# Performance work log

Measured on AMD Instinct MI355X. Metric: run time of the kernel, lower is better.

The kernel has to match this reference:

```python
import jax, jax.numpy as jnp
from jax import lax
import numpy as np


def _conv(x, w, b, pad):
    y = lax.conv_general_dilated(x, w, (1, 1), [(pad, pad), (pad, pad)],
                                 dimension_numbers=('NCHW', 'OIHW', 'NCHW'))
    return y + b[None, :, None, None]


def _bn(x, g, b, eps=1e-5):
    # training-mode batchnorm (batch statistics, biased variance) like torch default
    m = jnp.mean(x, (0, 2, 3), keepdims=True)
    v = jnp.mean((x - m) ** 2, (0, 2, 3), keepdims=True)
    return g[None, :, None, None] * (x - m) * lax.rsqrt(v + eps) + b[None, :, None, None]


def _maxpool2(x):
    return lax.reduce_window(x, -jnp.inf, lax.max, (1, 1, 2, 2), (1, 1, 2, 2), 'VALID')


def _power_features(x):
    # vectorized version of the per-image FFT + radial-bin histogram mean
    B, _, H, W = x.shape
    cy, cx = H // 2, W // 2
    yy, xx = jnp.meshgrid(jnp.arange(H), jnp.arange(W), indexing='ij')
    r = jnp.sqrt((xx - cx).astype(jnp.float32) ** 2 + (yy - cy).astype(jnp.float32) ** 2)
    max_r = min(H, W) // 2
    NB = 32
    r_bins = jnp.linspace(0.0, float(max_r), NB + 1)
    # bin j covers [r_bins[j], r_bins[j+1]) exactly as the torch mask
    idx = jnp.searchsorted(r_bins, r.ravel(), side='right') - 1
    valid = (idx >= 0) & (idx < NB)
    seg = jnp.where(valid, idx, NB)  # dump out-of-range into bin NB
    counts = jax.ops.segment_sum(valid.astype(jnp.float32), seg, NB + 1)[:NB]
    ps = jnp.abs(jnp.fft.fft2(x[:, 0])) ** 2  # [B,H,W]
    psf = ps.reshape(B, -1) * valid.astype(ps.dtype)[None, :]
    sums = jax.vmap(lambda p: jax.ops.segment_sum(p, seg, NB + 1))(psf)[:, :NB]
    radial = jnp.where(counts > 0, sums / jnp.maximum(counts, 1.0), 0.0)
    return jnp.log(radial + 1e-10)  # [B,32]


def reference(x, cw1, cb1, g1, bb1, cw2, cb2, g2, bb2, cw3, cb3, g3, bb3,
              cw4, cb4, g4, bb4, pcw, pcb, pg, pbb,
              pw1, pb1, pw2, pb2, pw3, pb3,
              fw1, fb1, fw2, fb2, fw3, fb3, fw4, fb4):
    h = jax.nn.relu(_bn(_conv(x, cw1, cb1, 2), g1, bb1)); h = _maxpool2(h)
    h = jax.nn.relu(_bn(_conv(h, cw2, cb2, 2), g2, bb2)); h = _maxpool2(h)
    h = jax.nn.relu(_bn(_conv(h, cw3, cb3, 1), g3, bb3)); h = _maxpool2(h)
    h = jax.nn.relu(_bn(_conv(h, cw4, cb4, 1), g4, bb4))        # [B,256,32,32]
    p = jax.nn.relu(_bn(_conv(h, pcw, pcb, 1), pg, pbb))        # [B,128,32,32]
    # adaptive avg pool (4,4): exact 8x8 windows, stride 8
    p = lax.reduce_window(p, 0.0, lax.add, (1, 1, 8, 8), (1, 1, 8, 8), 'VALID') / 64.0
    flat = p.reshape(p.shape[0], -1)  # [B,2048]
    pf = _power_features(x)           # [B,32]
    pf = jax.nn.relu(pf @ pw1.T + pb1)
    pf = jax.nn.relu(pf @ pw2.T + pb2)
    pf = jax.nn.relu(pf @ pw3.T + pb3)  # [B,64]
    c = jnp.concatenate([flat, pf], axis=1)  # [B,2112]
    c = jax.nn.relu(c @ fw1.T + fb1)
    c = jax.nn.relu(c @ fw2.T + fb2)
    c = jax.nn.relu(c @ fw3.T + fb3)
    return c @ fw4.T + fb4  # [B,2]


def setup_inputs() -> dict:
    key = jax.random.key(0)
    ki = iter(jax.random.split(key, 40))

    def W(shape):
        fan_in = int(np.prod(shape[1:]))
        return jax.random.normal(next(ki), shape, jnp.float32) / np.sqrt(fan_in)

    d = {'x': jax.random.normal(next(ki), (16, 1, 256, 256), jnp.float32)}
    convs = [('cw1', 'cb1', 'g1', 'bb1', (32, 1, 5, 5)),
             ('cw2', 'cb2', 'g2', 'bb2', (64, 32, 5, 5)),
             ('cw3', 'cb3', 'g3', 'bb3', (128, 64, 3, 3)),
             ('cw4', 'cb4', 'g4', 'bb4', (256, 128, 3, 3)),
             ('pcw', 'pcb', 'pg', 'pbb', (128, 256, 3, 3))]
    for wn, bn, gn, ben, s in convs:
        d[wn] = W(s); d[bn] = jnp.zeros(s[0], jnp.float32)
        d[gn] = jnp.ones(s[0], jnp.float32); d[ben] = jnp.zeros(s[0], jnp.float32)
    lins = [('pw1', 'pb1', (256, 32)), ('pw2', 'pb2', (128, 256)), ('pw3', 'pb3', (64, 128)),
            ('fw1', 'fb1', (512, 2112)), ('fw2', 'fb2', (256, 512)),
            ('fw3', 'fb3', (128, 256)), ('fw4', 'fb4', (2, 128))]
    for wn, bn, s in lins:
        d[wn] = W(s); d[bn] = jnp.zeros(s[0], jnp.float32)
    return d
```

## Files before the change

kernel.cpp:

```cpp
#include <hip/hip_runtime.h>
#include <math.h>


#define PI2F 6.283185307179586f

typedef _Float16 half8 __attribute__((ext_vector_type(8)));
typedef _Float16 half4v __attribute__((ext_vector_type(4)));
typedef float f32x4 __attribute__((ext_vector_type(4)));


__device__ __forceinline__ int bitrev8(int x) {
  x = ((x & 0x0F) << 4) | ((x >> 4) & 0x0F);
  x = ((x & 0x33) << 2) | ((x >> 2) & 0x33);
  x = ((x & 0x55) << 1) | ((x >> 1) & 0x55);
  return x;
}

__global__ __launch_bounds__(64)
void fft_rows(const float* __restrict__ x, float2* __restrict__ out) {
  __shared__ float2 s[256];
  __shared__ float2 tw[128];
  int blk = blockIdx.x;
  const float* rowp = x + (size_t)blk * 256;
  int t = threadIdx.x;
  for (int i = t; i < 128; i += 64) {
    float sn, cs;
    sincosf(-(PI2F / 256.f) * (float)i, &sn, &cs);
    tw[i] = make_float2(cs, sn);
  }
  #pragma unroll
  for (int e = 0; e < 4; ++e) {
    int i = t + (e << 6);
    s[bitrev8(i)] = make_float2(rowp[i], 0.f);
  }
  __syncthreads();
  #pragma unroll
  for (int st = 1; st <= 8; ++st) {
    int half = 1 << (st - 1);
    #pragma unroll
    for (int j = 0; j < 2; ++j) {
      int bf = t + (j << 6);
      int pos = bf & (half - 1);
      int grp = bf >> (st - 1);
      int i0 = (grp << st) | pos;
      int i1 = i0 + half;
      int k = pos << (8 - st);
      float cs = tw[k].x, sn = tw[k].y;
      float2 a = s[i0], b = s[i1];
      float tr = cs * b.x - sn * b.y;
      float ti = cs * b.y + sn * b.x;
      s[i0] = make_float2(a.x + tr, a.y + ti);
      s[i1] = make_float2(a.x - tr, a.y - ti);
    }
    __syncthreads();
  }
  float2* op = out + (size_t)blk * 256;
  #pragma unroll
  for (int e = 0; e < 4; ++e) { int i = t + (e << 6); op[i] = s[i]; }
}

__device__ __forceinline__ int radial_bin(int r2) {
  int j = (int)(sqrtf((float)r2) * 0.25f);
  while ((j + 1) * (j + 1) * 16 <= r2) ++j;
  while (j > 0 && j * j * 16 > r2) --j;
  return j;
}

__global__ __launch_bounds__(256)
void fft_cols_radial_v2(const float2* __restrict__ f, float* __restrict__ radial) {
  __shared__ float2 s[8][258];
  __shared__ float2 tw[128];
  __shared__ float bins[8][32];
  int b = blockIdx.x >> 5;
  int col0 = (blockIdx.x & 31) * 8;
  int t = threadIdx.x;
  for (int i = t; i < 128; i += 256) {
    float sn, cs;
    sincosf(-(PI2F / 256.f) * (float)i, &sn, &cs);
    tw[i] = make_float2(cs, sn);
  }
  ((float*)bins)[t] = 0.f;
  for (int idx = t; idx < 2048; idx += 256) {
    int row = idx >> 3, c = idx & 7;
    s[c][bitrev8(row)] = f[(size_t)b * 65536 + row * 256 + col0 + c];
  }
  __syncthreads();
  int c = t >> 5, l = t & 31;
  float2* sc = &s[c][0];
  #pragma unroll
  for (int st = 1; st <= 8; ++st) {
    int half = 1 << (st - 1);
    #pragma unroll
    for (int j = 0; j < 4; ++j) {
      int bf = l + (j << 5);
      int pos = bf & (half - 1);
      int grp = bf >> (st - 1);
      int i0 = (grp << st) | pos;
      int i1 = i0 + half;
      int k = pos << (8 - st);
      float cs = tw[k].x, sn = tw[k].y;
      float2 a = sc[i0], bb = sc[i1];
      float tr = cs * bb.x - sn * bb.y;
      float ti = cs * bb.y + sn * bb.x;
      sc[i0] = make_float2(a.x + tr, a.y + ti);
      sc[i1] = make_float2(a.x - tr, a.y - ti);
    }
    __syncthreads();
  }
  int dx = col0 + c - 128;
  #pragma unroll
  for (int e = 0; e < 8; ++e) {
    int i = l * 8 + e;
    float2 v = sc[i];
    float ps = v.x * v.x + v.y * v.y;
    int dy = i - 128;
    int r2 = dx * dx + dy * dy;
    if (r2 < 16384) atomicAdd(&bins[c][radial_bin(r2)], ps);
  }
  __syncthreads();
  if (t < 32) {
    float s0 = bins[0][t] + bins[1][t] + bins[2][t] + bins[3][t] +
               bins[4][t] + bins[5][t] + bins[6][t] + bins[7][t];
    atomicAdd(&radial[b * 32 + t], s0);
  }
}

__device__ __forceinline__ int isqrt_(int v) {
  int r = (int)sqrtf((float)v);
  while (r * r > v) --r;
  while ((r + 1) * (r + 1) <= v) ++r;
  return r;
}

__global__ __launch_bounds__(256)
void radial_finalize_v3(const float* __restrict__ radial, float* __restrict__ pf0) {
  __shared__ int red[4];
  __shared__ int cnt_s;
  int j = blockIdx.x, t = threadIdx.x;
  int dy = t - 128;
  int lo = 16 * j * j, hi = 16 * (j + 1) * (j + 1);
  int d2 = dy * dy;
  int cnt = 0;
  int tHi = hi - 1 - d2;
  if (tHi >= 0) {
    int rHi = isqrt_(tHi);
    int nHi = min(rHi, 127) + min(rHi, 128) + 1;
    int nLo = 0;
    int tLo = lo - 1 - d2;
    if (tLo >= 0) { int rLo = isqrt_(tLo); nLo = min(rLo, 127) + min(rLo, 128) + 1; }
    cnt = nHi - nLo;
  }
  #pragma unroll
  for (int off = 32; off > 0; off >>= 1) cnt += __shfl_down(cnt, off);
  if ((t & 63) == 0) red[t >> 6] = cnt;
  __syncthreads();
  if (t == 0) cnt_s = red[0] + red[1] + red[2] + red[3];
  __syncthreads();
  if (t < 16) {
    float cf = (float)cnt_s;
    float sum = radial[t * 32 + j];
    float val = cf > 0.f ? sum / fmaxf(cf, 1.f) : 0.f;
    pf0[t * 32 + j] = logf(val + 1e-10f);
  }
}


__global__ __launch_bounds__(256)
void wtrans_all(const float* __restrict__ cw2, const float* __restrict__ cw3,
                const float* __restrict__ cw4, const float* __restrict__ pcw,
                _Float16* __restrict__ wb2, _Float16* __restrict__ wb3,
                _Float16* __restrict__ wb4, _Float16* __restrict__ wbp) {
  int blk = blockIdx.x;
  const float* src; _Float16* dst; int COUT, CIN, KK, i;
  if (blk < 200)       { src = cw2; dst = wb2; COUT = 64;  CIN = 32;  KK = 25; i = blk * 256; }
  else if (blk < 488)  { src = cw3; dst = wb3; COUT = 128; CIN = 64;  KK = 9;  i = (blk - 200) * 256; }
  else if (blk < 1640) { src = cw4; dst = wb4; COUT = 256; CIN = 128; KK = 9;  i = (blk - 488) * 256; }
  else                 { src = pcw; dst = wbp; COUT = 128; CIN = 256; KK = 9;  i = (blk - 1640) * 256; }
  i += threadIdx.x;
  if (i >= COUT * CIN * KK) return;
  int ci = i % CIN;
  int r = i / CIN;
  int co = r % COUT;
  int tap = r / COUT;
  dst[i] = (_Float16)src[((size_t)co * CIN + ci) * KK + tap];
}


__device__ __forceinline__ void load16(float* d, const float* p) {
  f32x4 v0 = *(const f32x4*)(p);
  f32x4 v1 = *(const f32x4*)(p + 4);
  f32x4 v2 = *(const f32x4*)(p + 8);
  f32x4 v3 = *(const f32x4*)(p + 12);
  #pragma unroll
  for (int e = 0; e < 4; ++e) { d[e] = v0[e]; d[4+e] = v1[e]; d[8+e] = v2[e]; d[12+e] = v3[e]; }
}

__global__ __launch_bounds__(256)
void conv1_stats_v3(const float* __restrict__ x, const float* __restrict__ w,
                    float* __restrict__ stats) {
  __shared__ float lds[12 * 264];
  __shared__ float r1[4][32], r2[4][32];
  int t = threadIdx.x;
  int y0 = blockIdx.x * 8, n = blockIdx.y;
  const float* xp = x + (size_t)n * 65536;
  for (int i = t; i < 12 * 264; i += 256) {
    int r = i / 264, cc = i % 264;
    int gy = y0 + r - 2, gx = cc - 4;
    lds[i] = (gy >= 0 && gy < 256 && gx >= 0 && gx < 256) ? xp[gy * 256 + gx] : 0.f;
  }
  __syncthreads();
  int c = t & 31, xg = t >> 5;
  float wreg[25];
  #pragma unroll
  for (int k = 0; k < 25; ++k) wreg[k] = w[c * 25 + k];
  float s1 = 0.f, s2 = 0.f;
  for (int strip = 0; strip < 4; ++strip) {
    int px0 = xg * 8 + strip * 64;
    float f[5][16];
    #pragma unroll
    for (int rr = 0; rr < 4; ++rr) load16(f[rr], &lds[rr * 264 + px0]);
    #pragma unroll
    for (int r = 0; r < 8; ++r) {
      load16(f[(r + 4) % 5], &lds[(r + 4) * 264 + px0]);
      f32x4 A = {0.f, 0.f, 0.f, 0.f}, B = {0.f, 0.f, 0.f, 0.f};
      #pragma unroll
      for (int ky = 0; ky < 5; ++ky) {
        const float* fr = f[(r + ky) % 5];
        #pragma unroll
        for (int kx = 0; kx < 5; ++kx) {
          float wv = wreg[ky * 5 + kx];
          f32x4 ia = {fr[2 + kx], fr[3 + kx], fr[4 + kx], fr[5 + kx]};
          f32x4 ib = {fr[6 + kx], fr[7 + kx], fr[8 + kx], fr[9 + kx]};
          A += wv * ia; B += wv * ib;
        }
      }
      s1 += A[0] + A[1] + A[2] + A[3] + B[0] + B[1] + B[2] + B[3];
      s2 += A[0]*A[0] + A[1]*A[1] + A[2]*A[2] + A[3]*A[3]
          + B[0]*B[0] + B[1]*B[1] + B[2]*B[2] + B[3]*B[3];
    }
  }
  s1 += __shfl_down(s1, 32);
  s2 += __shfl_down(s2, 32);
  if ((t & 63) < 32) { r1[t >> 6][t & 31] = s1; r2[t >> 6][t & 31] = s2; }
  __syncthreads();
  if (t < 32) {
    atomicAdd(&stats[t],      r1[0][t] + r1[1][t] + r1[2][t] + r1[3][t]);
    atomicAdd(&stats[32 + t], r2[0][t] + r2[1][t] + r2[2][t] + r2[3][t]);
  }
}

__global__ __launch_bounds__(256)
void conv1_apply_v3(const float* __restrict__ x, const float* __restrict__ w,
                    const float* __restrict__ stats, const float* __restrict__ g,
                    const float* __restrict__ bb, _Float16* __restrict__ pool1) {
  __shared__ float lds[6 * 264];
  int t = threadIdx.x;
  int py = blockIdx.x, n = blockIdx.y;
  const float* xp = x + (size_t)n * 65536;
  for (int i = t; i < 6 * 264; i += 256) {
    int r = i / 264, cc = i % 264;
    int gy = 2 * py + r - 2, gx = cc - 4;
    lds[i] = (gy >= 0 && gy < 256 && gx >= 0 && gx < 256) ? xp[gy * 256 + gx] : 0.f;
  }
  __syncthreads();
  int c = t & 31, xg = t >> 5;
  float wreg[25];
  #pragma unroll
  for (int k = 0; k < 25; ++k) wreg[k] = w[c * 25 + k];
  float mean = stats[c] * (1.f / 1048576.f);
  float var  = stats[32 + c] * (1.f / 1048576.f) - mean * mean;
  float sc = g[c] / sqrtf(var + 1e-5f);
  float sh = bb[c] - mean * sc;
  for (int iter = 0; iter < 4; ++iter) {
    int p0 = xg * 4 + iter * 32;
    float f[6][16];
    #pragma unroll
    for (int rr = 0; rr < 6; ++rr) load16(f[rr], &lds[rr * 264 + 2 * p0]);
    f32x4 acc[2][2];
    #pragma unroll
    for (int sy = 0; sy < 2; ++sy)
      #pragma unroll
      for (int h = 0; h < 2; ++h) acc[sy][h] = (f32x4){0.f, 0.f, 0.f, 0.f};
    #pragma unroll
    for (int sy = 0; sy < 2; ++sy)
      #pragma unroll
      for (int ky = 0; ky < 5; ++ky) {
        const float* fr = f[sy + ky];
        #pragma unroll
        for (int kx = 0; kx < 5; ++kx) {
          float wv = wreg[ky * 5 + kx];
          f32x4 ia = {fr[2 + kx], fr[3 + kx], fr[4 + kx], fr[5 + kx]};
          f32x4 ib = {fr[6 + kx], fr[7 + kx], fr[8 + kx], fr[9 + kx]};
          acc[sy][0] += wv * ia; acc[sy][1] += wv * ib;
        }
      }
    #pragma unroll
    for (int pp = 0; pp < 4; ++pp) {
      float v00 = acc[0][(2*pp) >> 2][(2*pp) & 3];
      float v01 = acc[0][(2*pp+1) >> 2][(2*pp+1) & 3];
      float v10 = acc[1][(2*pp) >> 2][(2*pp) & 3];
      float v11 = acc[1][(2*pp+1) >> 2][(2*pp+1) & 3];
      float m = fmaxf(fmaxf(v00, v01), fmaxf(v10, v11));
      pool1[(((size_t)n * 128 + py) * 128 + p0 + pp) * 32 + c] =
          (_Float16)fmaxf(m * sc + sh, 0.f);
    }
  }
}


template <int CIN, int COUT, int H, int W, int K, int TH, int TW, int CW,
          int COT, int PT, int SLAB, int POOL>
__global__ __launch_bounds__(256)
void conv_mfma3(const _Float16* __restrict__ in, const _Float16* __restrict__ wb,
                _Float16* __restrict__ out, float* __restrict__ stats,
                size_t minoff) {
  constexpr int P = K / 2, R = TH + 2 * P, XW = TW + 2 * P, PIX = R * XW;
  constexpr int TAPS = K * K, CSP = SLAB + 8;
  constexpr int NCC = SLAB / 32, NPH = CIN / SLAB, SUBS = SLAB / 8;
  constexpr int PW = 4 / CW, COB = CW * 16 * COT;
  static_assert(TH * TW == PW * 16 * PT, "pos tile mismatch");
  static_assert(TW == 16, "row-per-fragment requires TW=16");
  static_assert(!POOL || (PT % 2 == 0), "pool needs even PT");
  __shared__ _Float16 lds[PIX * CSP];
  __shared__ float sst[2][COB];
  int t = threadIdx.x;
  int lane = t & 63, wv = t >> 6;
  int lane15 = lane & 15, quad = lane >> 4;
  constexpr int WT = W / TW;
  int x0 = (blockIdx.x % WT) * TW, y0 = (blockIdx.x / WT) * TH;
  int coB = blockIdx.y * COB;
  int nb = blockIdx.z;
  int co_off = (wv % CW) * (16 * COT);
  int rowbase = (wv / CW) * PT;

  for (int i = t; i < 2 * COB; i += 256) ((float*)sst)[i] = 0.f;

  f32x4 acc[COT][PT];
  #pragma unroll
  for (int ct = 0; ct < COT; ++ct)
    #pragma unroll
    for (int pt = 0; pt < PT; ++pt)
      #pragma unroll
      for (int e = 0; e < 4; ++e) acc[ct][pt][e] = 0.f;

  int bbase[PT];
  #pragma unroll
  for (int pt = 0; pt < PT; ++pt)
    bbase[pt] = ((rowbase + pt) * XW + lane15) * CSP + quad * 8;
  const _Float16* aptr[COT];
  #pragma unroll
  for (int ct = 0; ct < COT; ++ct)
    aptr[ct] = wb + (size_t)(coB + co_off + ct * 16 + lane15) * CIN + quad * 8;

  const _Float16* inb = in + (size_t)nb * H * W * CIN;

  #pragma unroll
  for (int ph = 0; ph < NPH; ++ph) {
    constexpr int ITEMS = PIX * SUBS;
    for (int i = t; i < ITEMS; i += 256) {
      int sub = i % SUBS, pix = i / SUBS;
      int r = pix / XW, xx = pix % XW;
      int gy = y0 + r - P, gx = x0 + xx - P;
      half8 v;
      #pragma unroll
      for (int j = 0; j < 8; ++j) v[j] = (_Float16)0.f;
      if (gy >= 0 && gy < H && gx >= 0 && gx < W)
        v = *(const half8*)(inb + ((size_t)gy * W + gx) * CIN + ph * SLAB + sub * 8);
      *(half8*)(&lds[pix * CSP + sub * 8]) = v;
    }
    __syncthreads();
    #pragma unroll
    for (int cc = 0; cc < NCC; ++cc) {
      #pragma unroll
      for (int tap = 0; tap < TAPS; ++tap) {
        int ky = tap / K, kx = tap % K;
        half8 a[COT], b[PT];
        #pragma unroll
        for (int ct = 0; ct < COT; ++ct)
          a[ct] = *(const half8*)(aptr[ct] + (size_t)tap * COUT * CIN +
                                  ph * SLAB + cc * 32);
        #pragma unroll
        for (int pt = 0; pt < PT; ++pt)
          b[pt] = *(const half8*)(&lds[bbase[pt] + (ky * XW + kx) * CSP + cc * 32]);
        #pragma unroll
        for (int ct = 0; ct < COT; ++ct)
          #pragma unroll
          for (int pt = 0; pt < PT; ++pt)
            acc[ct][pt] = __builtin_amdgcn_mfma_f32_16x16x32_f16(
                a[ct], b[pt], acc[ct][pt], 0, 0, 0);
      }
    }
    if (ph + 1 < NPH) __syncthreads();
  }

  if (POOL) {
    #pragma unroll
    for (int ct = 0; ct < COT; ++ct)
      #pragma unroll
      for (int pp = 0; pp < PT; pp += 2) {
        half4v hmax, hmin;
        #pragma unroll
        for (int e = 0; e < 4; ++e) {
          float vmx = fmaxf(acc[ct][pp][e], acc[ct][pp + 1][e]);
          float vmn = fminf(acc[ct][pp][e], acc[ct][pp + 1][e]);
          float omx = fmaxf(vmx, __shfl_xor(vmx, 1));
          float omn = fminf(vmn, __shfl_xor(vmn, 1));
          hmax[e] = (_Float16)omx; hmin[e] = (_Float16)omn;
        }
        if ((lane15 & 1) == 0) {
          int co = coB + co_off + ct * 16 + quad * 4;
          int prow = (y0 + rowbase + pp) >> 1;
          int pcol = (x0 >> 1) + (lane15 >> 1);
          size_t idx = (((size_t)nb * (H / 2) + prow) * (W / 2) + pcol) * COUT + co;
          *(half4v*)(out + idx) = hmax;
          *(half4v*)(out + minoff + idx) = hmin;
        }
      }
  } else {
    #pragma unroll
    for (int ct = 0; ct < COT; ++ct)
      #pragma unroll
      for (int pt = 0; pt < PT; ++pt) {
        int co = coB + co_off + ct * 16 + quad * 4;
        int y = y0 + rowbase + pt, x = x0 + lane15;
        _Float16* op = out + (((size_t)nb * H + y) * W + x) * COUT + co;
        half4v h;
        #pragma unroll
        for (int e = 0; e < 4; ++e) h[e] = (_Float16)acc[ct][pt][e];
        *(half4v*)op = h;
      }
  }

  #pragma unroll
  for (int ct = 0; ct < COT; ++ct)
    #pragma unroll
    for (int e = 0; e < 4; ++e) {
      float sv = 0.f, sq = 0.f;
      #pragma unroll
      for (int pt = 0; pt < PT; ++pt) {
        float v = acc[ct][pt][e];
        sv += v; sq += v * v;
      }
      sv += __shfl_xor(sv, 1); sq += __shfl_xor(sq, 1);
      sv += __shfl_xor(sv, 2); sq += __shfl_xor(sq, 2);
      sv += __shfl_xor(sv, 4); sq += __shfl_xor(sq, 4);
      sv += __shfl_xor(sv, 8); sq += __shfl_xor(sq, 8);
      if (lane15 == 0) {
        int cl = co_off + ct * 16 + quad * 4 + e;
        atomicAdd(&sst[0][cl], sv);
        atomicAdd(&sst[1][cl], sq);
      }
    }
  __syncthreads();
  float* st = stats + (blockIdx.x & 7) * 2 * COUT;
  for (int i = t; i < COB; i += 256) {
    atomicAdd(&st[coB + i], sst[0][i]);
    atomicAdd(&st[COUT + coB + i], sst[1][i]);
  }
}


__device__ __forceinline__ void bn_coeff(const float* stats, int C, int c,
                                         float invN, const float* g,
                                         const float* bb, float* sc, float* sh) {
  float s1 = 0.f, s2 = 0.f;
  #pragma unroll
  for (int s = 0; s < 8; ++s) {
    s1 += stats[s * 2 * C + c];
    s2 += stats[s * 2 * C + C + c];
  }
  float mean = s1 * invN;
  float var  = s2 * invN - mean * mean;
  float k = g[c] / sqrtf(var + 1e-5f);
  *sc = k; *sh = bb[c] - mean * k;
}

__global__ __launch_bounds__(256)
void bn_relu_sel(const _Float16* __restrict__ raw, const float* __restrict__ stats,
                 const float* __restrict__ g, const float* __restrict__ bb,
                 _Float16* __restrict__ out, int C, int total, float invN,
                 size_t minoff) {
  __shared__ float scs[256], shs[256];
  int t = threadIdx.x, n = blockIdx.y;
  for (int c = t; c < C; c += 256) bn_coeff(stats, C, c, invN, g, bb, &scs[c], &shs[c]);
  __syncthreads();
  for (int i = blockIdx.x * 256 + t; i < total; i += gridDim.x * 256) {
    int c = i % C;
    size_t idx = (size_t)n * total + i;
    float sc = scs[c];
    float v = sc >= 0.f ? (float)raw[idx] : (float)raw[minoff + idx];
    out[idx] = (_Float16)fmaxf(sc * v + shs[c], 0.f);
  }
}

__global__ __launch_bounds__(256)
void bn_relu_h16(const _Float16* __restrict__ x, const float* __restrict__ stats,
                 const float* __restrict__ g, const float* __restrict__ bb,
                 _Float16* __restrict__ out, int C, int HW, float invN) {
  __shared__ float scs[256], shs[256];
  int t = threadIdx.x;
  int n = blockIdx.y;
  for (int c = t; c < C; c += 256) bn_coeff(stats, C, c, invN, g, bb, &scs[c], &shs[c]);
  __syncthreads();
  int total = HW * C;
  int chunk = total / gridDim.x;
  int base = blockIdx.x * chunk;
  const _Float16* xp = x + (size_t)n * total;
  _Float16* op = out + (size_t)n * total;
  for (int i = base + t; i < base + chunk; i += 256) {
    int c = i % C;
    op[i] = (_Float16)fmaxf((float)xp[i] * scs[c] + shs[c], 0.f);
  }
}

__global__ __launch_bounds__(256)
void bn_avgpool_concat(const _Float16* __restrict__ x, const float* __restrict__ stats,
                       const float* __restrict__ g, const float* __restrict__ bb,
                       float* __restrict__ concat, float invN) {
  __shared__ float scs[128], shs[128];
  int t = threadIdx.x;
  int n = blockIdx.x;
  for (int c = t; c < 128; c += 256) bn_coeff(stats, 128, c, invN, g, bb, &scs[c], &shs[c]);
  __syncthreads();
  for (int i = t; i < 2048; i += 256) {
    int c = i & 127, opix = i >> 7;
    int py = opix >> 2, px = opix & 3;
    float sc = scs[c], sh = shs[c];
    float s = 0.f;
    for (int yy = 0; yy < 8; ++yy)
      for (int xx = 0; xx < 8; ++xx)
        s += fmaxf((float)x[(((size_t)n * 32 + py * 8 + yy) * 32 + px * 8 + xx) * 128 + c] * sc + sh, 0.f);
    concat[(size_t)n * 2112 + c * 16 + opix] = s * (1.f / 64.f);
  }
}


__global__ __launch_bounds__(64)
void linear_k(const float* __restrict__ in, const float* __restrict__ w,
              const float* __restrict__ bias, float* __restrict__ out,
              int I, int in_stride, int out_stride, int relu) {
  int o = blockIdx.x, b = blockIdx.y;
  int lane = threadIdx.x;
  const float* ip = in + (size_t)b * in_stride;
  const float* wp = w + (size_t)o * I;
  float acc = 0.f;
  for (int i = lane; i < I; i += 64) acc += ip[i] * wp[i];
  #pragma unroll
  for (int off = 32; off > 0; off >>= 1) acc += __shfl_down(acc, off);
  if (lane == 0) {
    float v = acc + bias[o];
    if (relu) v = fmaxf(v, 0.f);
    out[(size_t)b * out_stride + o] = v;
  }
}

__global__ __launch_bounds__(256)
void pf_mlp(const float* __restrict__ pf0,
            const float* __restrict__ pw1, const float* __restrict__ pb1,
            const float* __restrict__ pw2, const float* __restrict__ pb2,
            const float* __restrict__ pw3, const float* __restrict__ pb3,
            float* __restrict__ concat) {
  __shared__ float a0[32], a1[256], a2[128];
  int b = blockIdx.x, t = threadIdx.x;
  if (t < 32) a0[t] = pf0[b * 32 + t];
  __syncthreads();
  {
    float s = pb1[t];
    for (int i = 0; i < 32; ++i) s += pw1[t * 32 + i] * a0[i];
    a1[t] = fmaxf(s, 0.f);
  }
  __syncthreads();
  if (t < 128) {
    float s = pb2[t];
    for (int i = 0; i < 256; ++i) s += pw2[t * 256 + i] * a1[i];
    a2[t] = fmaxf(s, 0.f);
  }
  __syncthreads();
  if (t < 64) {
    float s = pb3[t];
    for (int i = 0; i < 128; ++i) s += pw3[t * 128 + i] * a2[i];
    concat[(size_t)b * 2112 + 2048 + t] = fmaxf(s, 0.f);
  }
}

__global__ __launch_bounds__(256)
void fc_tail(const float* __restrict__ fc1o,
             const float* __restrict__ fw2, const float* __restrict__ fb2,
             const float* __restrict__ fw3, const float* __restrict__ fb3,
             const float* __restrict__ fw4, const float* __restrict__ fb4,
             float* __restrict__ out) {
  __shared__ float a1[512], a2[256], a3[128];
  int b = blockIdx.x, t = threadIdx.x;
  a1[t] = fc1o[b * 512 + t];
  a1[t + 256] = fc1o[b * 512 + t + 256];
  __syncthreads();
  {
    float s = fb2[t];
    for (int i = 0; i < 512; ++i) s += fw2[t * 512 + i] * a1[i];
    a2[t] = fmaxf(s, 0.f);
  }
  __syncthreads();
  if (t < 128) {
    float s = fb3[t];
    for (int i = 0; i < 256; ++i) s += fw3[t * 256 + i] * a2[i];
    a3[t] = fmaxf(s, 0.f);
  }
  __syncthreads();
  if (t < 2) {
    float s = fb4[t];
    for (int i = 0; i < 128; ++i) s += fw4[t * 128 + i] * a3[i];
    out[b * 2 + t] = s;
  }
}


extern "C" void kernel_launch(void* const* d_in, const int* in_sizes, int n_in,
                              void* d_out, int out_size, void* d_ws, size_t ws_size,
                              hipStream_t stream) {
  (void)in_sizes; (void)n_in; (void)out_size; (void)ws_size;
  const float* x   = (const float*)d_in[0];
  const float* cw1 = (const float*)d_in[1];
  const float* g1  = (const float*)d_in[3];
  const float* bb1 = (const float*)d_in[4];
  const float* cw2 = (const float*)d_in[5];
  const float* g2  = (const float*)d_in[7];
  const float* bb2 = (const float*)d_in[8];
  const float* cw3 = (const float*)d_in[9];
  const float* g3  = (const float*)d_in[11];
  const float* bb3 = (const float*)d_in[12];
  const float* cw4 = (const float*)d_in[13];
  const float* g4  = (const float*)d_in[15];
  const float* bb4 = (const float*)d_in[16];
  const float* pcw = (const float*)d_in[17];
  const float* pg  = (const float*)d_in[19];
  const float* pbb = (const float*)d_in[20];
  const float* pw1 = (const float*)d_in[21];
  const float* pb1 = (const float*)d_in[22];
  const float* pw2 = (const float*)d_in[23];
  const float* pb2 = (const float*)d_in[24];
  const float* pw3 = (const float*)d_in[25];
  const float* pb3 = (const float*)d_in[26];
  const float* fw1 = (const float*)d_in[27];
  const float* fb1 = (const float*)d_in[28];
  const float* fw2 = (const float*)d_in[29];
  const float* fb2 = (const float*)d_in[30];
  const float* fw3 = (const float*)d_in[31];
  const float* fb3 = (const float*)d_in[32];
  const float* fw4 = (const float*)d_in[33];
  const float* fb4 = (const float*)d_in[34];

  char* base = (char*)d_ws;
  float2*    fftbuf   = (float2*)(base + 0);
  _Float16*  pool2raw = (_Float16*)(base + 0);
  _Float16*  pool3raw = (_Float16*)(base + 0);
  _Float16*  conv4raw = (_Float16*)(base + 0);
  _Float16*  pconvo   = (_Float16*)(base + 8388608);
  _Float16*  pool1    = (_Float16*)(base + 16777216);
  _Float16*  pool2    = (_Float16*)(base + 33554432);
  _Float16*  pool3    = (_Float16*)(base + 41943040);
  _Float16*  act4     = (_Float16*)(base + 46137344);
  _Float16*  wb2      = (_Float16*)(base + 54525952);
  _Float16*  wb3      = (_Float16*)(base + 54628352);
  _Float16*  wb4      = (_Float16*)(base + 54775808);
  _Float16*  wbp      = (_Float16*)(base + 55365632);
  float*     zbase    = (float*)(base + 55955456);
  float*     stats1   = zbase;
  float*     stats2   = zbase + 64;
  float*     stats3   = zbase + 1088;
  float*     stats4   = zbase + 3136;
  float*     stats5   = zbase + 7232;
  float*     radial   = zbase + 9280;
  float*     pf0      = (float*)(base + 55994624);
  float*     concat   = (float*)(base + 55996672);
  float*     fc1o     = (float*)(base + 56131840);

  hipMemsetAsync(zbase, 0, 9792 * sizeof(float), stream);

  wtrans_all<<<2792, 256, 0, stream>>>(cw2, cw3, cw4, pcw, wb2, wb3, wb4, wbp);

  fft_rows<<<4096, 64, 0, stream>>>(x, fftbuf);
  fft_cols_radial_v2<<<512, 256, 0, stream>>>(fftbuf, radial);
  radial_finalize_v3<<<32, 256, 0, stream>>>(radial, pf0);
  pf_mlp<<<16, 256, 0, stream>>>(pf0, pw1, pb1, pw2, pb2, pw3, pb3, concat);

  conv1_stats_v3<<<dim3(32, 16), 256, 0, stream>>>(x, cw1, stats1);
  conv1_apply_v3<<<dim3(128, 16), 256, 0, stream>>>(x, cw1, stats1, g1, bb1, pool1);

  conv_mfma3<32, 64, 128, 128, 5, 16, 16, 1, 4, 4, 32, 1>
      <<<dim3(64, 1, 16), 256, 0, stream>>>(pool1, wb2, pool2raw, stats2, 4194304);
  bn_relu_sel<<<dim3(64, 16), 256, 0, stream>>>(
      pool2raw, stats2, g2, bb2, pool2, 64, 262144, 1.f / 262144.f, 4194304);

  conv_mfma3<64, 128, 64, 64, 3, 8, 16, 2, 4, 4, 64, 1>
      <<<dim3(32, 1, 16), 256, 0, stream>>>(pool2, wb3, pool3raw, stats3, 2097152);
  bn_relu_sel<<<dim3(32, 16), 256, 0, stream>>>(
      pool3raw, stats3, g3, bb3, pool3, 128, 131072, 1.f / 65536.f, 2097152);

  conv_mfma3<128, 256, 32, 32, 3, 4, 16, 2, 4, 2, 128, 0>
      <<<dim3(16, 2, 16), 256, 0, stream>>>(pool3, wb4, conv4raw, stats4, 0);
  bn_relu_h16<<<dim3(8, 16), 256, 0, stream>>>(
      conv4raw, stats4, g4, bb4, act4, 256, 1024, 1.f / 16384.f);

  conv_mfma3<256, 128, 32, 32, 3, 4, 16, 2, 2, 2, 128, 0>
      <<<dim3(16, 2, 16), 256, 0, stream>>>(act4, wbp, pconvo, stats5, 0);
  bn_avgpool_concat<<<16, 256, 0, stream>>>(pconvo, stats5, pg, pbb, concat, 1.f / 16384.f);

  linear_k<<<dim3(512, 16), 64, 0, stream>>>(concat, fw1, fb1, fc1o, 2112, 2112, 512, 1);
  fc_tail<<<16, 256, 0, stream>>>(fc1o, fw2, fb2, fw3, fb3, fw4, fb4, (float*)d_out);
}
```

Measured before the change: 466.9 us.

## Fuse BN-ReLU into next conv's input load and single-pass conv1 with max/min pooling

Conv1 is now computed once: its stats kernel also writes pooled max and min raw outputs, which replaces the separate apply pass that recomputed the convolution. Each MFMA conv applies the previous layer's batchnorm and ReLU while loading its input tile, choosing the max or min pooled value by the sign of the scale. This removes the standalone bn_relu kernels and their activation round trips through memory. Conv1 stats are split across 8 atomic slots to reduce contention. Some tile and grid shapes change (conv2 tile, conv4 COT), and bn_avgpool_concat is parallelised over more blocks. The cost is extra per-element BN math in the conv load path and a second min-buffer read.

```diff
diff --git a/kernel.cpp b/kernel.cpp
--- a/kernel.cpp
+++ b/kernel.cpp
@@ -196,8 +196,9 @@
 }
 
 __global__ __launch_bounds__(256)
-void conv1_stats_v3(const float* __restrict__ x, const float* __restrict__ w,
-                    float* __restrict__ stats) {
+void conv1_fused(const float* __restrict__ x, const float* __restrict__ w,
+                 _Float16* __restrict__ praw, size_t minoff,
+                 float* __restrict__ stats) {
   __shared__ float lds[12 * 264];
   __shared__ float r1[4][32], r2[4][32];
   int t = threadIdx.x;
@@ -219,6 +220,7 @@
     float f[5][16];
     #pragma unroll
     for (int rr = 0; rr < 4; ++rr) load16(f[rr], &lds[rr * 264 + px0]);
+    float pmax[4], pmin[4];
     #pragma unroll
     for (int r = 0; r < 8; ++r) {
       load16(f[(r + 4) % 5], &lds[(r + 4) * 264 + px0]);
@@ -237,6 +239,24 @@
       s1 += A[0] + A[1] + A[2] + A[3] + B[0] + B[1] + B[2] + B[3];
       s2 += A[0]*A[0] + A[1]*A[1] + A[2]*A[2] + A[3]*A[3]
           + B[0]*B[0] + B[1]*B[1] + B[2]*B[2] + B[3]*B[3];
+      float cm[4], cn[4];
+      cm[0] = fmaxf(A[0], A[1]); cn[0] = fminf(A[0], A[1]);
+      cm[1] = fmaxf(A[2], A[3]); cn[1] = fminf(A[2], A[3]);
+      cm[2] = fmaxf(B[0], B[1]); cn[2] = fminf(B[0], B[1]);
+      cm[3] = fmaxf(B[2], B[3]); cn[3] = fminf(B[2], B[3]);
+      if ((r & 1) == 0) {
+        #pragma unroll
+        for (int k = 0; k < 4; ++k) { pmax[k] = cm[k]; pmin[k] = cn[k]; }
+      } else {
+        int prow = (y0 + r) >> 1;
+        int pc0 = px0 >> 1;
+        #pragma unroll
+        for (int k = 0; k < 4; ++k) {
+          size_t idx = (((size_t)n * 128 + prow) * 128 + pc0 + k) * 32 + c;
+          praw[idx] = (_Float16)fmaxf(pmax[k], cm[k]);
+          praw[minoff + idx] = (_Float16)fminf(pmin[k], cn[k]);
+        }
+      }
     }
   }
   s1 += __shfl_down(s1, 32);
@@ -244,84 +264,31 @@
   if ((t & 63) < 32) { r1[t >> 6][t & 31] = s1; r2[t >> 6][t & 31] = s2; }
   __syncthreads();
   if (t < 32) {
-    atomicAdd(&stats[t],      r1[0][t] + r1[1][t] + r1[2][t] + r1[3][t]);
-    atomicAdd(&stats[32 + t], r2[0][t] + r2[1][t] + r2[2][t] + r2[3][t]);
-  }
-}
-
-__global__ __launch_bounds__(256)
-void conv1_apply_v3(const float* __restrict__ x, const float* __restrict__ w,
-                    const float* __restrict__ stats, const float* __restrict__ g,
-                    const float* __restrict__ bb, _Float16* __restrict__ pool1) {
-  __shared__ float lds[6 * 264];
-  int t = threadIdx.x;
-  int py = blockIdx.x, n = blockIdx.y;
-  const float* xp = x + (size_t)n * 65536;
-  for (int i = t; i < 6 * 264; i += 256) {
-    int r = i / 264, cc = i % 264;
-    int gy = 2 * py + r - 2, gx = cc - 4;
-    lds[i] = (gy >= 0 && gy < 256 && gx >= 0 && gx < 256) ? xp[gy * 256 + gx] : 0.f;
-  }
-  __syncthreads();
-  int c = t & 31, xg = t >> 5;
-  float wreg[25];
-  #pragma unroll
-  for (int k = 0; k < 25; ++k) wreg[k] = w[c * 25 + k];
-  float mean = stats[c] * (1.f / 1048576.f);
-  float var  = stats[32 + c] * (1.f / 1048576.f) - mean * mean;
-  float sc = g[c] / sqrtf(var + 1e-5f);
-  float sh = bb[c] - mean * sc;
-  for (int iter = 0; iter < 4; ++iter) {
-    int p0 = xg * 4 + iter * 32;
-    float f[6][16];
-    #pragma unroll
-    for (int rr = 0; rr < 6; ++rr) load16(f[rr], &lds[rr * 264 + 2 * p0]);
-    f32x4 acc[2][2];
-    #pragma unroll
-    for (int sy = 0; sy < 2; ++sy)
-      #pragma unroll
-      for (int h = 0; h < 2; ++h) acc[sy][h] = (f32x4){0.f, 0.f, 0.f, 0.f};
-    #pragma unroll
-    for (int sy = 0; sy < 2; ++sy)
-      #pragma unroll
-      for (int ky = 0; ky < 5; ++ky) {
-        const float* fr = f[sy + ky];
-        #pragma unroll
-        for (int kx = 0; kx < 5; ++kx) {
-          float wv = wreg[ky * 5 + kx];
-          f32x4 ia = {fr[2 + kx], fr[3 + kx], fr[4 + kx], fr[5 + kx]};
-          f32x4 ib = {fr[6 + kx], fr[7 + kx], fr[8 + kx], fr[9 + kx]};
-          acc[sy][0] += wv * ia; acc[sy][1] += wv * ib;
-        }
-      }
-    #pragma unroll
-    for (int pp = 0; pp < 4; ++pp) {
-      float v00 = acc[0][(2*pp) >> 2][(2*pp) & 3];
-      float v01 = acc[0][(2*pp+1) >> 2][(2*pp+1) & 3];
-      float v10 = acc[1][(2*pp) >> 2][(2*pp) & 3];
-      float v11 = acc[1][(2*pp+1) >> 2][(2*pp+1) & 3];
-      float m = fmaxf(fmaxf(v00, v01), fmaxf(v10, v11));
-      pool1[(((size_t)n * 128 + py) * 128 + p0 + pp) * 32 + c] =
-          (_Float16)fmaxf(m * sc + sh, 0.f);
-    }
+    float* st = stats + (blockIdx.x & 7) * 64;
+    atomicAdd(&st[t],      r1[0][t] + r1[1][t] + r1[2][t] + r1[3][t]);
+    atomicAdd(&st[32 + t], r2[0][t] + r2[1][t] + r2[2][t] + r2[3][t]);
   }
 }
 
 
 template <int CIN, int COUT, int H, int W, int K, int TH, int TW, int CW,
-          int COT, int PT, int SLAB, int POOL>
-__global__ __launch_bounds__(256)
-void conv_mfma3(const _Float16* __restrict__ in, const _Float16* __restrict__ wb,
-                _Float16* __restrict__ out, float* __restrict__ stats,
-                size_t minoff) {
+          int COT, int PT, int SLAB, int INPOOL, int OUTPOOL>
+__global__ __launch_bounds__(256)
+void conv_mfma4(const _Float16* __restrict__ in, size_t in_minoff,
+                const _Float16* __restrict__ wb,
+                _Float16* __restrict__ out, size_t out_minoff,
+                const float* __restrict__ instats, const float* __restrict__ ing,
+                const float* __restrict__ inbb, float in_invN,
+                float* __restrict__ stats) {
   constexpr int P = K / 2, R = TH + 2 * P, XW = TW + 2 * P, PIX = R * XW;
   constexpr int TAPS = K * K, CSP = SLAB + 8;
   constexpr int NCC = SLAB / 32, NPH = CIN / SLAB, SUBS = SLAB / 8;
   constexpr int PW = 4 / CW, COB = CW * 16 * COT;
   static_assert(TH * TW == PW * 16 * PT, "pos tile mismatch");
   static_assert(TW == 16, "row-per-fragment requires TW=16");
-  static_assert(!POOL || (PT % 2 == 0), "pool needs even PT");
+  static_assert(!OUTPOOL || (PT % 2 == 0), "pool needs even PT");
   __shared__ _Float16 lds[PIX * CSP];
+  __shared__ float inscs[CIN], inshs[CIN];
   __shared__ float sst[2][COB];
   int t = threadIdx.x;
   int lane = t & 63, wv = t >> 6;
@@ -334,6 +301,19 @@
   int rowbase = (wv / CW) * PT;
 
   for (int i = t; i < 2 * COB; i += 256) ((float*)sst)[i] = 0.f;
+  for (int c = t; c < CIN; c += 256) {
+    float s1 = 0.f, s2 = 0.f;
+    #pragma unroll
+    for (int s = 0; s < 8; ++s) {
+      s1 += instats[s * 2 * CIN + c];
+      s2 += instats[s * 2 * CIN + CIN + c];
+    }
+    float mean = s1 * in_invN;
+    float var  = s2 * in_invN - mean * mean;
+    float k = ing[c] / sqrtf(var + 1e-5f);
+    inscs[c] = k; inshs[c] = inbb[c] - mean * k;
+  }
+  __syncthreads();
 
   f32x4 acc[COT][PT];
   #pragma unroll
@@ -352,7 +332,7 @@
   for (int ct = 0; ct < COT; ++ct)
     aptr[ct] = wb + (size_t)(coB + co_off + ct * 16 + lane15) * CIN + quad * 8;
 
-  const _Float16* inb = in + (size_t)nb * H * W * CIN;
+  const size_t ibase = (size_t)nb * H * W * CIN;
 
   #pragma unroll
   for (int ph = 0; ph < NPH; ++ph) {
@@ -361,11 +341,29 @@
       int sub = i % SUBS, pix = i / SUBS;
       int r = pix / XW, xx = pix % XW;
       int gy = y0 + r - P, gx = x0 + xx - P;
+      int ch = ph * SLAB + sub * 8;
       half8 v;
       #pragma unroll
       for (int j = 0; j < 8; ++j) v[j] = (_Float16)0.f;
-      if (gy >= 0 && gy < H && gx >= 0 && gx < W)
-        v = *(const half8*)(inb + ((size_t)gy * W + gx) * CIN + ph * SLAB + sub * 8);
+      if (gy >= 0 && gy < H && gx >= 0 && gx < W) {
+        size_t off = ibase + ((size_t)gy * W + gx) * CIN + ch;
+        half8 vmx = *(const half8*)(in + off);
+        if (INPOOL) {
+          half8 vmn = *(const half8*)(in + in_minoff + off);
+          #pragma unroll
+          for (int j = 0; j < 8; ++j) {
+            float sc = inscs[ch + j];
+            float xv = sc >= 0.f ? (float)vmx[j] : (float)vmn[j];
+            v[j] = (_Float16)fmaxf(sc * xv + inshs[ch + j], 0.f);
+          }
+        } else {
+          #pragma unroll
+          for (int j = 0; j < 8; ++j) {
+            float sc = inscs[ch + j];
+            v[j] = (_Float16)fmaxf(sc * (float)vmx[j] + inshs[ch + j], 0.f);
+          }
+        }
+      }
       *(half8*)(&lds[pix * CSP + sub * 8]) = v;
     }
     __syncthreads();
@@ -393,7 +391,7 @@
     if (ph + 1 < NPH) __syncthreads();
   }
 
-  if (POOL) {
+  if (OUTPOOL) {
     #pragma unroll
     for (int ct = 0; ct < COT; ++ct)
       #pragma unroll
@@ -413,7 +411,7 @@
           int pcol = (x0 >> 1) + (lane15 >> 1);
           size_t idx = (((size_t)nb * (H / 2) + prow) * (W / 2) + pcol) * COUT + co;
           *(half4v*)(out + idx) = hmax;
-          *(half4v*)(out + minoff + idx) = hmin;
+          *(half4v*)(out + out_minoff + idx) = hmin;
         }
       }
   } else {
@@ -460,78 +458,36 @@
 }
 
 
-__device__ __forceinline__ void bn_coeff(const float* stats, int C, int c,
-                                         float invN, const float* g,
-                                         const float* bb, float* sc, float* sh) {
-  float s1 = 0.f, s2 = 0.f;
-  #pragma unroll
-  for (int s = 0; s < 8; ++s) {
-    s1 += stats[s * 2 * C + c];
-    s2 += stats[s * 2 * C + C + c];
-  }
-  float mean = s1 * invN;
-  float var  = s2 * invN - mean * mean;
-  float k = g[c] / sqrtf(var + 1e-5f);
-  *sc = k; *sh = bb[c] - mean * k;
-}
-
-__global__ __launch_bounds__(256)
-void bn_relu_sel(const _Float16* __restrict__ raw, const float* __restrict__ stats,
-                 const float* __restrict__ g, const float* __restrict__ bb,
-                 _Float16* __restrict__ out, int C, int total, float invN,
-                 size_t minoff) {
-  __shared__ float scs[256], shs[256];
-  int t = threadIdx.x, n = blockIdx.y;
-  for (int c = t; c < C; c += 256) bn_coeff(stats, C, c, invN, g, bb, &scs[c], &shs[c]);
-  __syncthreads();
-  for (int i = blockIdx.x * 256 + t; i < total; i += gridDim.x * 256) {
-    int c = i % C;
-    size_t idx = (size_t)n * total + i;
-    float sc = scs[c];
-    float v = sc >= 0.f ? (float)raw[idx] : (float)raw[minoff + idx];
-    out[idx] = (_Float16)fmaxf(sc * v + shs[c], 0.f);
-  }
-}
-
-__global__ __launch_bounds__(256)
-void bn_relu_h16(const _Float16* __restrict__ x, const float* __restrict__ stats,
-                 const float* __restrict__ g, const float* __restrict__ bb,
-                 _Float16* __restrict__ out, int C, int HW, float invN) {
-  __shared__ float scs[256], shs[256];
-  int t = threadIdx.x;
-  int n = blockIdx.y;
-  for (int c = t; c < C; c += 256) bn_coeff(stats, C, c, invN, g, bb, &scs[c], &shs[c]);
-  __syncthreads();
-  int total = HW * C;
-  int chunk = total / gridDim.x;
-  int base = blockIdx.x * chunk;
-  const _Float16* xp = x + (size_t)n * total;
-  _Float16* op = out + (size_t)n * total;
-  for (int i = base + t; i < base + chunk; i += 256) {
-    int c = i % C;
-    op[i] = (_Float16)fmaxf((float)xp[i] * scs[c] + shs[c], 0.f);
-  }
-}
-
 __global__ __launch_bounds__(256)
 void bn_avgpool_concat(const _Float16* __restrict__ x, const float* __restrict__ stats,
                        const float* __restrict__ g, const float* __restrict__ bb,
                        float* __restrict__ concat, float invN) {
   __shared__ float scs[128], shs[128];
   int t = threadIdx.x;
-  int n = blockIdx.x;
-  for (int c = t; c < 128; c += 256) bn_coeff(stats, 128, c, invN, g, bb, &scs[c], &shs[c]);
-  __syncthreads();
-  for (int i = t; i < 2048; i += 256) {
-    int c = i & 127, opix = i >> 7;
-    int py = opix >> 2, px = opix & 3;
-    float sc = scs[c], sh = shs[c];
-    float s = 0.f;
-    for (int yy = 0; yy < 8; ++yy)
-      for (int xx = 0; xx < 8; ++xx)
-        s += fmaxf((float)x[(((size_t)n * 32 + py * 8 + yy) * 32 + px * 8 + xx) * 128 + c] * sc + sh, 0.f);
-    concat[(size_t)n * 2112 + c * 16 + opix] = s * (1.f / 64.f);
-  }
+  int n = blockIdx.y;
+  for (int c = t; c < 128; c += 256) {
+    float s1 = 0.f, s2 = 0.f;
+    #pragma unroll
+    for (int s = 0; s < 8; ++s) {
+      s1 += stats[s * 256 + c];
+      s2 += stats[s * 256 + 128 + c];
+    }
+    float mean = s1 * invN;
+    float var  = s2 * invN - mean * mean;
+    float k = g[c] / sqrtf(var + 1e-5f);
+    scs[c] = k; shs[c] = bb[c] - mean * k;
+  }
+  __syncthreads();
+  int i = blockIdx.x * 256 + t;
+  int c = i & 127, opix = i >> 7;
+  int py = opix >> 2, px = opix & 3;
+  float sc = scs[c], sh = shs[c];
+  float s = 0.f;
+  for (int yy = 0; yy < 8; ++yy)
+    #pragma unroll
+    for (int xx = 0; xx < 8; ++xx)
+      s += fmaxf((float)x[(((size_t)n * 32 + py * 8 + yy) * 32 + px * 8 + xx) * 128 + c] * sc + sh, 0.f);
+  concat[(size_t)n * 2112 + c * 16 + opix] = s * (1.f / 64.f);
 }
 
 
@@ -650,31 +606,28 @@
   const float* fb4 = (const float*)d_in[34];
 
   char* base = (char*)d_ws;
-  float2*    fftbuf   = (float2*)(base + 0);
-  _Float16*  pool2raw = (_Float16*)(base + 0);
-  _Float16*  pool3raw = (_Float16*)(base + 0);
-  _Float16*  conv4raw = (_Float16*)(base + 0);
-  _Float16*  pconvo   = (_Float16*)(base + 8388608);
-  _Float16*  pool1    = (_Float16*)(base + 16777216);
-  _Float16*  pool2    = (_Float16*)(base + 33554432);
-  _Float16*  pool3    = (_Float16*)(base + 41943040);
-  _Float16*  act4     = (_Float16*)(base + 46137344);
-  _Float16*  wb2      = (_Float16*)(base + 54525952);
-  _Float16*  wb3      = (_Float16*)(base + 54628352);
-  _Float16*  wb4      = (_Float16*)(base + 54775808);
-  _Float16*  wbp      = (_Float16*)(base + 55365632);
-  float*     zbase    = (float*)(base + 55955456);
-  float*     stats1   = zbase;
-  float*     stats2   = zbase + 64;
-  float*     stats3   = zbase + 1088;
-  float*     stats4   = zbase + 3136;
-  float*     stats5   = zbase + 7232;
-  float*     radial   = zbase + 9280;
-  float*     pf0      = (float*)(base + 55994624);
-  float*     concat   = (float*)(base + 55996672);
-  float*     fc1o     = (float*)(base + 56131840);
-
-  hipMemsetAsync(zbase, 0, 9792 * sizeof(float), stream);
+  _Float16* pool1raw = (_Float16*)(base + 0);
+  _Float16* pool3raw = (_Float16*)(base + 0);
+  _Float16* pconvo   = (_Float16*)(base + 8388608);
+  _Float16* pool2raw = (_Float16*)(base + 33554432);
+  float2*   fftbuf   = (float2*)(base + 33554432);
+  _Float16* conv4raw = (_Float16*)(base + 33554432);
+  _Float16* wb2      = (_Float16*)(base + 50331648);
+  _Float16* wb3      = (_Float16*)(base + 50434048);
+  _Float16* wb4      = (_Float16*)(base + 50581504);
+  _Float16* wbp      = (_Float16*)(base + 51171328);
+  float*    zbase    = (float*)(base + 51761152);
+  float*    stats1   = zbase;
+  float*    stats2   = zbase + 512;
+  float*    stats3   = zbase + 1536;
+  float*    stats4   = zbase + 3584;
+  float*    stats5   = zbase + 7680;
+  float*    radial   = zbase + 9728;
+  float*    pf0      = (float*)(base + 51802112);
+  float*    concat   = (float*)(base + 51804160);
+  float*    fc1o     = (float*)(base + 51939328);
+
+  hipMemsetAsync(zbase, 0, 10240 * sizeof(float), stream);
 
   wtrans_all<<<2792, 256, 0, stream>>>(cw2, cw3, cw4, pcw, wb2, wb3, wb4, wbp);
 
@@ -683,27 +636,29 @@
   radial_finalize_v3<<<32, 256, 0, stream>>>(radial, pf0);
   pf_mlp<<<16, 256, 0, stream>>>(pf0, pw1, pb1, pw2, pb2, pw3, pb3, concat);
 
-  conv1_stats_v3<<<dim3(32, 16), 256, 0, stream>>>(x, cw1, stats1);
-  conv1_apply_v3<<<dim3(128, 16), 256, 0, stream>>>(x, cw1, stats1, g1, bb1, pool1);
-
-  conv_mfma3<32, 64, 128, 128, 5, 16, 16, 1, 4, 4, 32, 1>
-      <<<dim3(64, 1, 16), 256, 0, stream>>>(pool1, wb2, pool2raw, stats2, 4194304);
-  bn_relu_sel<<<dim3(64, 16), 256, 0, stream>>>(
-      pool2raw, stats2, g2, bb2, pool2, 64, 262144, 1.f / 262144.f, 4194304);
-
-  conv_mfma3<64, 128, 64, 64, 3, 8, 16, 2, 4, 4, 64, 1>
-      <<<dim3(32, 1, 16), 256, 0, stream>>>(pool2, wb3, pool3raw, stats3, 2097152);
-  bn_relu_sel<<<dim3(32, 16), 256, 0, stream>>>(
-      pool3raw, stats3, g3, bb3, pool3, 128, 131072, 1.f / 65536.f, 2097152);
-
-  conv_mfma3<128, 256, 32, 32, 3, 4, 16, 2, 4, 2, 128, 0>
-      <<<dim3(16, 2, 16), 256, 0, stream>>>(pool3, wb4, conv4raw, stats4, 0);
-  bn_relu_h16<<<dim3(8, 16), 256, 0, stream>>>(
-      conv4raw, stats4, g4, bb4, act4, 256, 1024, 1.f / 16384.f);
-
-  conv_mfma3<256, 128, 32, 32, 3, 4, 16, 2, 2, 2, 128, 0>
-      <<<dim3(16, 2, 16), 256, 0, stream>>>(act4, wbp, pconvo, stats5, 0);
-  bn_avgpool_concat<<<16, 256, 0, stream>>>(pconvo, stats5, pg, pbb, concat, 1.f / 16384.f);
+  conv1_fused<<<dim3(32, 16), 256, 0, stream>>>(x, cw1, pool1raw, 8388608, stats1);
+
+  conv_mfma4<32, 64, 128, 128, 5, 8, 16, 2, 2, 4, 32, 1, 1>
+      <<<dim3(128, 1, 16), 256, 0, stream>>>(
+      pool1raw, 8388608, wb2, pool2raw, 4194304,
+      stats1, g1, bb1, 1.f / 1048576.f, stats2);
+
+  conv_mfma4<64, 128, 64, 64, 3, 8, 16, 2, 4, 4, 64, 1, 1>
+      <<<dim3(32, 1, 16), 256, 0, stream>>>(
+      pool2raw, 4194304, wb3, pool3raw, 2097152,
+      stats2, g2, bb2, 1.f / 262144.f, stats3);
+
+  conv_mfma4<128, 256, 32, 32, 3, 4, 16, 2, 2, 2, 128, 1, 0>
+      <<<dim3(16, 4, 16), 256, 0, stream>>>(
+      pool3raw, 2097152, wb4, conv4raw, 0,
+      stats3, g3, bb3, 1.f / 65536.f, stats4);
+
+  conv_mfma4<256, 128, 32, 32, 3, 4, 16, 2, 2, 2, 128, 0, 0>
+      <<<dim3(16, 2, 16), 256, 0, stream>>>(
+      conv4raw, 0, wbp, pconvo, 0,
+      stats4, g4, bb4, 1.f / 16384.f, stats5);
+  bn_avgpool_concat<<<dim3(8, 16), 256, 0, stream>>>(
+      pconvo, stats5, pg, pbb, concat, 1.f / 16384.f);
 
   linear_k<<<dim3(512, 16), 64, 0, stream>>>(concat, fw1, fb1, fc1o, 2112, 2112, 512, 1);
   fc_tail<<<16, 256, 0, stream>>>(fc1o, fw2, fb2, fw3, fb3, fw4, fb4, (float*)d_out);
```

New measurement: 408.5 us. 12.5% less time.
